# Kernel tuning notes

Measured on AMD Instinct MI355X. Metric: run time of the kernel, lower is better.

## Reference

```python
import jax, jax.numpy as jnp
import numpy as np

IN_DIM = 1024
OUT_DIM = 1024
QK_DIM = OUT_DIM // 4  # 256


def setup_inputs() -> dict:
    key = jax.random.key(0)
    kx, ky, kq, kk, kv = jax.random.split(key, 5)
    B, Sq, Sk = 16, 2048, 2048
    x = jax.random.normal(kx, (B, Sq, IN_DIM), dtype=jnp.float32)
    y = jax.random.normal(ky, (B, Sk, IN_DIM), dtype=jnp.float32)
    s = 1.0 / np.sqrt(IN_DIM)
    Wq = jax.random.normal(kq, (IN_DIM, QK_DIM), dtype=jnp.float32) * s
    Wk = jax.random.normal(kk, (IN_DIM, QK_DIM), dtype=jnp.float32) * s
    Wv = jax.random.normal(kv, (IN_DIM, OUT_DIM), dtype=jnp.float32) * s
    return {"x": x, "y": y, "Wq": Wq, "Wk": Wk, "Wv": Wv}


def reference(x, y, Wq, Wk, Wv):
    # q: [B,Sq,dk], k: [B,Sk,dk]
    q = jnp.einsum("bsd,dk->bsk", x, Wq)
    k = jnp.einsum("btd,dk->btk", y, Wk)
    # NOTE: original scales by out_dim**0.5, not qk dim
    scores = jnp.einsum("bsk,btk->bst", q, k) / jnp.sqrt(jnp.float32(OUT_DIM))
    attn = jax.nn.softmax(scores, axis=-1)
    v = jnp.einsum("btd,de->bte", y, Wv)
    out = jnp.einsum("bst,bte->bse", attn, v)
    return out + x
```

## Files before the change

kernel.cpp:

```cpp
#include <hip/hip_runtime.h>

typedef __attribute__((ext_vector_type(8))) short bf16x8;
typedef __attribute__((ext_vector_type(4))) short s16x4;
typedef __attribute__((ext_vector_type(4))) float f32x4;

#define MFMA16(a,b,c) __builtin_amdgcn_mfma_f32_16x16x32_bf16((a),(b),(c),0,0,0)

__device__ __forceinline__ unsigned short f2bf(float f) {
  unsigned int u = __float_as_uint(f);
  return (unsigned short)((u + 0x7fffu + ((u >> 16) & 1u)) >> 16);
}
__device__ __forceinline__ float bf2f(unsigned short u) {
  return __uint_as_float(((unsigned int)u) << 16);
}

__device__ __forceinline__ void gload16(const void* g, void* l) {
  __builtin_amdgcn_global_load_lds((const __attribute__((address_space(1))) void*)g,
                                   (__attribute__((address_space(3))) void*)l, 16, 0, 0);
}

__global__ __launch_bounds__(256) void cvt_bf16(const float* __restrict__ in,
                                                unsigned short* __restrict__ out, int n8) {
  for (int i = blockIdx.x * 256 + threadIdx.x; i < n8; i += gridDim.x * 256) {
    float4 a = ((const float4*)in)[2 * i];
    float4 b = ((const float4*)in)[2 * i + 1];
    s16x4 p0, p1;
    p0[0] = f2bf(a.x); p0[1] = f2bf(a.y); p0[2] = f2bf(a.z); p0[3] = f2bf(a.w);
    p1[0] = f2bf(b.x); p1[1] = f2bf(b.y); p1[2] = f2bf(b.z); p1[3] = f2bf(b.w);
    ((s16x4*)out)[2 * i] = p0;
    ((s16x4*)out)[2 * i + 1] = p1;
  }
}

__global__ __launch_bounds__(256) void tcvt(const float* __restrict__ W,
                                            unsigned short* __restrict__ Wt, int K, int N) {
  __shared__ float t[32][33];
  const int n0 = blockIdx.x * 32, k0 = blockIdx.y * 32;
  const int c = threadIdx.x & 31, r8 = threadIdx.x >> 5;
#pragma unroll
  for (int p = 0; p < 4; ++p) {
    int r = r8 + p * 8;
    t[r][c] = W[(size_t)(k0 + r) * N + n0 + c];
  }
  __syncthreads();
#pragma unroll
  for (int p = 0; p < 4; ++p) {
    int r = r8 + p * 8;
    Wt[(size_t)(n0 + r) * K + k0 + c] = f2bf(t[c][r]);
  }
}

__global__ __launch_bounds__(256) void proj_gemm(
    const unsigned short* __restrict__ A, const unsigned short* __restrict__ Bt,
    unsigned short* __restrict__ C, int N, int mode, float scale)
{
  __shared__ __align__(16) unsigned short As[2][4096];
  __shared__ __align__(16) unsigned short Bs[2][4096];
  const int tid = threadIdx.x, lane = tid & 63, w = tid >> 6;
  const int wr = w >> 1, wc = w & 1;
  const int lrow = lane & 15, lg = lane >> 4;
  const size_t bm = (size_t)blockIdx.x * 128;
  const size_t bn = (size_t)blockIdx.y * 128;
  const int rl = lane >> 2, cq = lane & 3;

  auto stage = [&](int kt, int buf) {
#pragma unroll
    for (int u = 0; u < 2; ++u) {
      int row = w * 32 + u * 16 + rl;
      gload16(A  + (bm + row) * 1024 + kt * 32 + cq * 8, &As[buf][(w * 32 + u * 16) * 32]);
      gload16(Bt + (bn + row) * 1024 + kt * 32 + cq * 8, &Bs[buf][(w * 32 + u * 16) * 32]);
    }
  };

  f32x4 acc[4][4] = {};
  stage(0, 0);
  __syncthreads();

  for (int kt = 0; kt < 32; ++kt) {
    const int cur = kt & 1;
    if (kt + 1 < 32) stage(kt + 1, cur ^ 1);
    bf16x8 af[4], bfr[4];
#pragma unroll
    for (int i = 0; i < 4; ++i)
      af[i] = *(const bf16x8*)&As[cur][(wr * 64 + i * 16 + lrow) * 32 + lg * 8];
#pragma unroll
    for (int j = 0; j < 4; ++j)
      bfr[j] = *(const bf16x8*)&Bs[cur][(wc * 64 + j * 16 + lrow) * 32 + lg * 8];
    __builtin_amdgcn_s_setprio(1);
#pragma unroll
    for (int i = 0; i < 4; ++i)
#pragma unroll
      for (int j = 0; j < 4; ++j)
        acc[i][j] = MFMA16(af[i], bfr[j], acc[i][j]);
    __builtin_amdgcn_s_setprio(0);
    __syncthreads();
  }

  const int orow0 = blockIdx.x * 128 + wr * 64;
  const int ocol0 = blockIdx.y * 128 + wc * 64;
  if (mode == 0) {
#pragma unroll
    for (int i = 0; i < 4; ++i)
#pragma unroll
      for (int j = 0; j < 4; ++j) {
        int col = ocol0 + j * 16 + lrow;
#pragma unroll
        for (int r = 0; r < 4; ++r) {
          int row = orow0 + i * 16 + lg * 4 + r;
          C[(size_t)row * N + col] = f2bf(acc[i][j][r] * scale);
        }
      }
  } else {
#pragma unroll
    for (int i = 0; i < 4; ++i) {
      int m0 = orow0 + i * 16 + lg * 4;
      int bb = m0 >> 11, t = m0 & 2047;
#pragma unroll
      for (int j = 0; j < 4; ++j) {
        int e = ocol0 + j * 16 + lrow;
        s16x4 pk;
#pragma unroll
        for (int r = 0; r < 4; ++r) pk[r] = (short)f2bf(acc[i][j][r]);
        *(s16x4*)(C + (size_t)bb * 2097152 + (size_t)e * 2048 + t) = pk;
      }
    }
  }
}

template<int NT, int NTIL, int MODE>
__global__ __launch_bounds__(512) void gemm8p(
    const unsigned short* __restrict__ Aall, const unsigned short* __restrict__ Ball,
    size_t abatch, size_t bbatch, int lda, int ldb,
    unsigned short* __restrict__ Cb, const float* __restrict__ X,
    float* __restrict__ Out, int b0, int nb)
{
  __shared__ __align__(16) unsigned short lds[65536];
  const int bid = blockIdx.x;
  const int bloc = bid % nb, tl = bid / nb;
  const int mtile = tl / NTIL, ntile = tl % NTIL;
  const int gb = b0 + bloc;
  const unsigned short* Ag = Aall + (MODE == 0 ? (size_t)gb : (size_t)bloc) * abatch
                                  + (size_t)mtile * 256 * lda;
  const unsigned short* Bg = Ball + (size_t)gb * bbatch + (size_t)ntile * 256 * ldb;

  const int tid = threadIdx.x, lane = tid & 63, w = tid >> 6;
  const int wm = w >> 2, wn = w & 3;
  const int lrow = lane & 15, lg = lane >> 4;
  char* lb = (char*)lds;

  auto stageU = [&](const unsigned short* G, int ld, int kofs, int ubyte) {
#pragma unroll
    for (int i = 0; i < 2; ++i) {
      int c = tid + 512 * i;
      int row = c >> 2, q = c & 3;
      int qs = q ^ ((row >> 1) & 3);
      gload16(G + (size_t)row * ld + kofs + qs * 8, lb + ubyte + c * 16);
    }
  };
  auto rdfrag = [&](int ubyte, int row) -> bf16x8 {
    return *(const bf16x8*)(lb + ubyte + row * 64 + ((lg ^ ((row >> 1) & 3)) << 4));
  };

  f32x4 acc[8][4] = {};
  bf16x8 af[8], bfr[2];

  stageU(Ag, lda, 0,  (0 * 2 + 0) * 16384);
  stageU(Bg, ldb, 0,  (1 * 2 + 0) * 16384);
  stageU(Ag, lda, 32, (2 * 2 + 0) * 16384);
  stageU(Bg, ldb, 32, (3 * 2 + 0) * 16384);
  stageU(Ag, lda, 64, (0 * 2 + 1) * 16384);
  stageU(Bg, ldb, 64, (1 * 2 + 1) * 16384);
  asm volatile("s_waitcnt vmcnt(8)" ::: "memory");
  __builtin_amdgcn_s_barrier();

  for (int T = 0; T < NT; ++T) {
    const int par = T & 1;
    const int a0b = (0 * 2 + par) * 16384, b0b = (1 * 2 + par) * 16384;
    const int a1b = (2 * 2 + par) * 16384, b1b = (3 * 2 + par) * 16384;

#pragma unroll
    for (int mf = 0; mf < 8; ++mf) af[mf] = rdfrag(a0b, wm * 128 + mf * 16 + lrow);
#pragma unroll
    for (int nf = 0; nf < 2; ++nf) bfr[nf] = rdfrag(b0b, wn * 64 + nf * 16 + lrow);
    if (T + 1 < NT) stageU(Ag, lda, (T + 1) * 64 + 32, (2 * 2 + ((T + 1) & 1)) * 16384);
    __builtin_amdgcn_s_barrier();
    asm volatile("s_waitcnt lgkmcnt(0)" ::: "memory");
    __builtin_amdgcn_sched_barrier(0);
    __builtin_amdgcn_s_setprio(1);
#pragma unroll
    for (int mf = 0; mf < 8; ++mf) {
      acc[mf][0] = MFMA16(af[mf], bfr[0], acc[mf][0]);
      acc[mf][1] = MFMA16(af[mf], bfr[1], acc[mf][1]);
    }
    __builtin_amdgcn_s_setprio(0);
    __builtin_amdgcn_s_barrier();

#pragma unroll
    for (int nf = 0; nf < 2; ++nf) bfr[nf] = rdfrag(b0b, wn * 64 + (nf + 2) * 16 + lrow);
    if (T + 1 < NT) stageU(Bg, ldb, (T + 1) * 64 + 32, (3 * 2 + ((T + 1) & 1)) * 16384);
    __builtin_amdgcn_s_barrier();
    asm volatile("s_waitcnt lgkmcnt(0)" ::: "memory");
    __builtin_amdgcn_sched_barrier(0);
    __builtin_amdgcn_s_setprio(1);
#pragma unroll
    for (int mf = 0; mf < 8; ++mf) {
      acc[mf][2] = MFMA16(af[mf], bfr[0], acc[mf][2]);
      acc[mf][3] = MFMA16(af[mf], bfr[1], acc[mf][3]);
    }
    __builtin_amdgcn_s_setprio(0);
    asm volatile("s_waitcnt vmcnt(8)" ::: "memory");
    __builtin_amdgcn_s_barrier();

#pragma unroll
    for (int mf = 0; mf < 8; ++mf) af[mf] = rdfrag(a1b, wm * 128 + mf * 16 + lrow);
#pragma unroll
    for (int nf = 0; nf < 2; ++nf) bfr[nf] = rdfrag(b1b, wn * 64 + (nf + 2) * 16 + lrow);
    if (T + 2 < NT) stageU(Ag, lda, (T + 2) * 64, (0 * 2 + par) * 16384);
    __builtin_amdgcn_s_barrier();
    asm volatile("s_waitcnt lgkmcnt(0)" ::: "memory");
    __builtin_amdgcn_sched_barrier(0);
    __builtin_amdgcn_s_setprio(1);
#pragma unroll
    for (int mf = 0; mf < 8; ++mf) {
      acc[mf][2] = MFMA16(af[mf], bfr[0], acc[mf][2]);
      acc[mf][3] = MFMA16(af[mf], bfr[1], acc[mf][3]);
    }
    __builtin_amdgcn_s_setprio(0);
    __builtin_amdgcn_s_barrier();

#pragma unroll
    for (int nf = 0; nf < 2; ++nf) bfr[nf] = rdfrag(b1b, wn * 64 + nf * 16 + lrow);
    if (T + 2 < NT) stageU(Bg, ldb, (T + 2) * 64, (1 * 2 + par) * 16384);
    __builtin_amdgcn_s_barrier();
    asm volatile("s_waitcnt lgkmcnt(0)" ::: "memory");
    __builtin_amdgcn_sched_barrier(0);
    __builtin_amdgcn_s_setprio(1);
#pragma unroll
    for (int mf = 0; mf < 8; ++mf) {
      acc[mf][0] = MFMA16(af[mf], bfr[0], acc[mf][0]);
      acc[mf][1] = MFMA16(af[mf], bfr[1], acc[mf][1]);
    }
    __builtin_amdgcn_s_setprio(0);
    asm volatile("s_waitcnt vmcnt(8)" ::: "memory");
    __builtin_amdgcn_s_barrier();
  }

  if (MODE == 0) {
    unsigned short* Cp = Cb + (size_t)bloc * 2048 * 2048;
#pragma unroll
    for (int mf = 0; mf < 8; ++mf)
#pragma unroll
      for (int r = 0; r < 4; ++r) {
        int row = mtile * 256 + wm * 128 + mf * 16 + lg * 4 + r;
#pragma unroll
        for (int nf = 0; nf < 4; ++nf) {
          int col = ntile * 256 + wn * 64 + nf * 16 + lrow;
          Cp[(size_t)row * 2048 + col] = f2bf(acc[mf][nf][r]);
        }
      }
  } else {
#pragma unroll
    for (int mf = 0; mf < 8; ++mf)
#pragma unroll
      for (int r = 0; r < 4; ++r) {
        int row = mtile * 256 + wm * 128 + mf * 16 + lg * 4 + r;
        const float* xr = X   + ((size_t)gb * 2048 + row) * 1024;
        float*      orp = Out + ((size_t)gb * 2048 + row) * 1024;
#pragma unroll
        for (int nf = 0; nf < 4; ++nf) {
          int col = ntile * 256 + wn * 64 + nf * 16 + lrow;
          orp[col] = acc[mf][nf][r] + xr[col];
        }
      }
  }
}

__global__ __launch_bounds__(256) void softmax_kernel(unsigned short* __restrict__ Sp) {
  const int row = blockIdx.x * 4 + (threadIdx.x >> 6);
  const int lane = threadIdx.x & 63;
  unsigned short* rp = Sp + (size_t)row * 2048;
  bf16x8 raw[4];
#pragma unroll
  for (int c = 0; c < 4; ++c) raw[c] = *(const bf16x8*)(rp + c * 512 + lane * 8);
  float v[32];
#pragma unroll
  for (int c = 0; c < 4; ++c)
#pragma unroll
    for (int j = 0; j < 8; ++j) v[c * 8 + j] = bf2f((unsigned short)raw[c][j]);
  float mx = v[0];
#pragma unroll
  for (int j = 1; j < 32; ++j) mx = fmaxf(mx, v[j]);
  mx = fmaxf(mx, __shfl_xor(mx, 1));
  mx = fmaxf(mx, __shfl_xor(mx, 2));
  mx = fmaxf(mx, __shfl_xor(mx, 4));
  mx = fmaxf(mx, __shfl_xor(mx, 8));
  mx = fmaxf(mx, __shfl_xor(mx, 16));
  mx = fmaxf(mx, __shfl_xor(mx, 32));
  float sum = 0.f;
#pragma unroll
  for (int j = 0; j < 32; ++j) { v[j] = __expf(v[j] - mx); sum += v[j]; }
  sum += __shfl_xor(sum, 1);
  sum += __shfl_xor(sum, 2);
  sum += __shfl_xor(sum, 4);
  sum += __shfl_xor(sum, 8);
  sum += __shfl_xor(sum, 16);
  sum += __shfl_xor(sum, 32);
  float inv = 1.0f / sum;
#pragma unroll
  for (int c = 0; c < 4; ++c) {
    bf16x8 pk;
#pragma unroll
    for (int j = 0; j < 8; ++j) pk[j] = (short)f2bf(v[c * 8 + j] * inv);
    *(bf16x8*)(rp + c * 512 + lane * 8) = pk;
  }
}

extern "C" void kernel_launch(void* const* d_in, const int* in_sizes, int n_in,
                              void* d_out, int out_size, void* d_ws, size_t ws_size,
                              hipStream_t stream) {
  (void)in_sizes; (void)n_in; (void)out_size;
  const float* x  = (const float*)d_in[0];
  const float* y  = (const float*)d_in[1];
  const float* Wq = (const float*)d_in[2];
  const float* Wk = (const float*)d_in[3];
  const float* Wv = (const float*)d_in[4];
  float* out = (float*)d_out;

  unsigned short* xb = (unsigned short*)d_out;
  unsigned short* yb = xb + (size_t)16 * 2048 * 1024;

  unsigned short* Wqt = (unsigned short*)d_ws;
  unsigned short* Wkt = Wqt + (size_t)256 * 1024;
  unsigned short* Wvt = Wkt + (size_t)256 * 1024;
  unsigned short* qws = Wvt + (size_t)1024 * 1024;
  unsigned short* kws = qws + (size_t)16 * 2048 * 256;
  unsigned short* vtw = kws + (size_t)16 * 2048 * 256;
  unsigned short* Sp  = vtw + (size_t)16 * 1024 * 2048;

  const size_t fixed_bytes = (size_t)(Sp - Wqt) * 2;
  const size_t s_batch_bytes = (size_t)2048 * 2048 * 2;
  int nb = 1;
  if      (ws_size >= fixed_bytes + 16 * s_batch_bytes) nb = 16;
  else if (ws_size >= fixed_bytes + 8  * s_batch_bytes) nb = 8;
  else if (ws_size >= fixed_bytes + 4  * s_batch_bytes) nb = 4;
  else if (ws_size >= fixed_bytes + 2  * s_batch_bytes) nb = 2;
  else nb = 1;

  const int n8 = (16 * 2048 * 1024) / 8;
  cvt_bf16<<<2048, 256, 0, stream>>>(x, xb, n8);
  cvt_bf16<<<2048, 256, 0, stream>>>(y, yb, n8);
  tcvt<<<dim3(8, 32),  256, 0, stream>>>(Wq, Wqt, 1024, 256);
  tcvt<<<dim3(8, 32),  256, 0, stream>>>(Wk, Wkt, 1024, 256);
  tcvt<<<dim3(32, 32), 256, 0, stream>>>(Wv, Wvt, 1024, 1024);

  proj_gemm<<<dim3(256, 2), 256, 0, stream>>>(xb, Wqt, qws, 256, 0, 0.03125f);
  proj_gemm<<<dim3(256, 2), 256, 0, stream>>>(yb, Wkt, kws, 256, 0, 1.0f);
  proj_gemm<<<dim3(256, 8), 256, 0, stream>>>(yb, Wvt, vtw, 1024, 2, 1.0f);

  for (int b0 = 0; b0 < 16; b0 += nb) {
    gemm8p<4, 8, 0><<<nb * 64, 512, 0, stream>>>(
        qws, kws, (size_t)2048 * 256, (size_t)2048 * 256, 256, 256,
        Sp, nullptr, nullptr, b0, nb);
    softmax_kernel<<<nb * 512, 256, 0, stream>>>(Sp);
    gemm8p<32, 4, 1><<<nb * 32, 512, 0, stream>>>(
        Sp, vtw, (size_t)2048 * 2048, (size_t)1024 * 2048, 2048, 2048,
        nullptr, x, out, b0, nb);
  }
}
```

Baseline: 532.9 us.

## Restructure GEMM main loop into 4-phase 4x4 MFMA blocks with prefetched fragments

```diff
diff --git a/kernel.cpp b/kernel.cpp
--- a/kernel.cpp
+++ b/kernel.cpp
@@ -127,8 +127,10 @@
   }
 }
 
+#define SBAR  do { __builtin_amdgcn_s_barrier(); __builtin_amdgcn_sched_barrier(0); } while (0)
+
 template<int NT, int NTIL, int MODE>
-__global__ __launch_bounds__(512) void gemm8p(
+__global__ __launch_bounds__(512) void gemm4p(
     const unsigned short* __restrict__ Aall, const unsigned short* __restrict__ Ball,
     size_t abatch, size_t bbatch, int lda, int ldb,
     unsigned short* __restrict__ Cb, const float* __restrict__ X,
@@ -162,7 +164,7 @@
   };
 
   f32x4 acc[8][4] = {};
-  bf16x8 af[8], bfr[2];
+  bf16x8 afA[4], afB[4], bfrA[4], bfrB[4];
 
   stageU(Ag, lda, 0,  (0 * 2 + 0) * 16384);
   stageU(Bg, ldb, 0,  (1 * 2 + 0) * 16384);
@@ -171,78 +173,80 @@
   stageU(Ag, lda, 64, (0 * 2 + 1) * 16384);
   stageU(Bg, ldb, 64, (1 * 2 + 1) * 16384);
   asm volatile("s_waitcnt vmcnt(8)" ::: "memory");
-  __builtin_amdgcn_s_barrier();
+  SBAR;
+#pragma unroll
+  for (int i = 0; i < 4; ++i) afA[i] = rdfrag(0, wm * 128 + i * 16 + lrow);
+#pragma unroll
+  for (int nf = 0; nf < 4; ++nf) bfrA[nf] = rdfrag(2 * 16384, wn * 64 + nf * 16 + lrow);
 
   for (int T = 0; T < NT; ++T) {
-    const int par = T & 1;
-    const int a0b = (0 * 2 + par) * 16384, b0b = (1 * 2 + par) * 16384;
-    const int a1b = (2 * 2 + par) * 16384, b1b = (3 * 2 + par) * 16384;
-
-#pragma unroll
-    for (int mf = 0; mf < 8; ++mf) af[mf] = rdfrag(a0b, wm * 128 + mf * 16 + lrow);
-#pragma unroll
-    for (int nf = 0; nf < 2; ++nf) bfr[nf] = rdfrag(b0b, wn * 64 + nf * 16 + lrow);
-    if (T + 1 < NT) stageU(Ag, lda, (T + 1) * 64 + 32, (2 * 2 + ((T + 1) & 1)) * 16384);
-    __builtin_amdgcn_s_barrier();
-    asm volatile("s_waitcnt lgkmcnt(0)" ::: "memory");
+    const int pc = T & 1, pn = (T + 1) & 1;
+    const int a0b = (0 * 2 + pc) * 16384, b0b = (1 * 2 + pc) * 16384;
+    const int a1b = (2 * 2 + pc) * 16384, b1b = (3 * 2 + pc) * 16384;
+    const int t1 = (T + 1 < NT) ? T + 1 : 0;
+    const int t2 = (T + 2 < NT) ? T + 2 : 0;
+
+#pragma unroll
+    for (int i = 0; i < 4; ++i) afB[i] = rdfrag(a0b, wm * 128 + (i + 4) * 16 + lrow);
+    stageU(Ag, lda, t1 * 64 + 32, (2 * 2 + pn) * 16384);
+    asm volatile("s_waitcnt lgkmcnt(4)" ::: "memory");
     __builtin_amdgcn_sched_barrier(0);
     __builtin_amdgcn_s_setprio(1);
 #pragma unroll
-    for (int mf = 0; mf < 8; ++mf) {
-      acc[mf][0] = MFMA16(af[mf], bfr[0], acc[mf][0]);
-      acc[mf][1] = MFMA16(af[mf], bfr[1], acc[mf][1]);
-    }
-    __builtin_amdgcn_s_setprio(0);
-    __builtin_amdgcn_s_barrier();
-
-#pragma unroll
-    for (int nf = 0; nf < 2; ++nf) bfr[nf] = rdfrag(b0b, wn * 64 + (nf + 2) * 16 + lrow);
-    if (T + 1 < NT) stageU(Bg, ldb, (T + 1) * 64 + 32, (3 * 2 + ((T + 1) & 1)) * 16384);
-    __builtin_amdgcn_s_barrier();
-    asm volatile("s_waitcnt lgkmcnt(0)" ::: "memory");
+    for (int mf = 0; mf < 4; ++mf)
+#pragma unroll
+      for (int nf = 0; nf < 4; ++nf)
+        acc[mf][nf] = MFMA16(afA[mf], bfrA[nf], acc[mf][nf]);
+    __builtin_amdgcn_s_setprio(0);
+    asm volatile("s_waitcnt vmcnt(6)" ::: "memory");
+    SBAR;
+
+#pragma unroll
+    for (int i = 0; i < 4; ++i) afA[i] = rdfrag(a1b, wm * 128 + i * 16 + lrow);
+#pragma unroll
+    for (int nf = 0; nf < 4; ++nf) bfrB[nf] = rdfrag(b1b, wn * 64 + nf * 16 + lrow);
+    stageU(Bg, ldb, t1 * 64 + 32, (3 * 2 + pn) * 16384);
+    asm volatile("s_waitcnt lgkmcnt(8)" ::: "memory");
     __builtin_amdgcn_sched_barrier(0);
     __builtin_amdgcn_s_setprio(1);
 #pragma unroll
-    for (int mf = 0; mf < 8; ++mf) {
-      acc[mf][2] = MFMA16(af[mf], bfr[0], acc[mf][2]);
-      acc[mf][3] = MFMA16(af[mf], bfr[1], acc[mf][3]);
-    }
-    __builtin_amdgcn_s_setprio(0);
-    asm volatile("s_waitcnt vmcnt(8)" ::: "memory");
-    __builtin_amdgcn_s_barrier();
-
-#pragma unroll
-    for (int mf = 0; mf < 8; ++mf) af[mf] = rdfrag(a1b, wm * 128 + mf * 16 + lrow);
-#pragma unroll
-    for (int nf = 0; nf < 2; ++nf) bfr[nf] = rdfrag(b1b, wn * 64 + (nf + 2) * 16 + lrow);
-    if (T + 2 < NT) stageU(Ag, lda, (T + 2) * 64, (0 * 2 + par) * 16384);
-    __builtin_amdgcn_s_barrier();
-    asm volatile("s_waitcnt lgkmcnt(0)" ::: "memory");
+    for (int mf = 0; mf < 4; ++mf)
+#pragma unroll
+      for (int nf = 0; nf < 4; ++nf)
+        acc[mf + 4][nf] = MFMA16(afB[mf], bfrA[nf], acc[mf + 4][nf]);
+    __builtin_amdgcn_s_setprio(0);
+    SBAR;
+
+#pragma unroll
+    for (int i = 0; i < 4; ++i) afB[i] = rdfrag(a1b, wm * 128 + (i + 4) * 16 + lrow);
+    stageU(Ag, lda, t2 * 64, (0 * 2 + pc) * 16384);
+    asm volatile("s_waitcnt lgkmcnt(4)" ::: "memory");
     __builtin_amdgcn_sched_barrier(0);
     __builtin_amdgcn_s_setprio(1);
 #pragma unroll
-    for (int mf = 0; mf < 8; ++mf) {
-      acc[mf][2] = MFMA16(af[mf], bfr[0], acc[mf][2]);
-      acc[mf][3] = MFMA16(af[mf], bfr[1], acc[mf][3]);
-    }
-    __builtin_amdgcn_s_setprio(0);
-    __builtin_amdgcn_s_barrier();
-
-#pragma unroll
-    for (int nf = 0; nf < 2; ++nf) bfr[nf] = rdfrag(b1b, wn * 64 + nf * 16 + lrow);
-    if (T + 2 < NT) stageU(Bg, ldb, (T + 2) * 64, (1 * 2 + par) * 16384);
-    __builtin_amdgcn_s_barrier();
-    asm volatile("s_waitcnt lgkmcnt(0)" ::: "memory");
+    for (int mf = 0; mf < 4; ++mf)
+#pragma unroll
+      for (int nf = 0; nf < 4; ++nf)
+        acc[mf][nf] = MFMA16(afA[mf], bfrB[nf], acc[mf][nf]);
+    __builtin_amdgcn_s_setprio(0);
+    asm volatile("s_waitcnt vmcnt(6)" ::: "memory");
+    SBAR;
+
+#pragma unroll
+    for (int i = 0; i < 4; ++i) afA[i] = rdfrag((0 * 2 + pn) * 16384, wm * 128 + i * 16 + lrow);
+#pragma unroll
+    for (int nf = 0; nf < 4; ++nf) bfrA[nf] = rdfrag((1 * 2 + pn) * 16384, wn * 64 + nf * 16 + lrow);
+    stageU(Bg, ldb, t2 * 64, (1 * 2 + pc) * 16384);
+    asm volatile("s_waitcnt lgkmcnt(8)" ::: "memory");
     __builtin_amdgcn_sched_barrier(0);
     __builtin_amdgcn_s_setprio(1);
 #pragma unroll
-    for (int mf = 0; mf < 8; ++mf) {
-      acc[mf][0] = MFMA16(af[mf], bfr[0], acc[mf][0]);
-      acc[mf][1] = MFMA16(af[mf], bfr[1], acc[mf][1]);
-    }
-    __builtin_amdgcn_s_setprio(0);
-    asm volatile("s_waitcnt vmcnt(8)" ::: "memory");
-    __builtin_amdgcn_s_barrier();
+    for (int mf = 0; mf < 4; ++mf)
+#pragma unroll
+      for (int nf = 0; nf < 4; ++nf)
+        acc[mf + 4][nf] = MFMA16(afB[mf], bfrB[nf], acc[mf + 4][nf]);
+    __builtin_amdgcn_s_setprio(0);
+    SBAR;
   }
 
   if (MODE == 0) {
@@ -358,11 +362,11 @@
   proj_gemm<<<dim3(256, 8), 256, 0, stream>>>(yb, Wvt, vtw, 1024, 2, 1.0f);
 
   for (int b0 = 0; b0 < 16; b0 += nb) {
-    gemm8p<4, 8, 0><<<nb * 64, 512, 0, stream>>>(
+    gemm4p<4, 8, 0><<<nb * 64, 512, 0, stream>>>(
         qws, kws, (size_t)2048 * 256, (size_t)2048 * 256, 256, 256,
         Sp, nullptr, nullptr, b0, nb);
     softmax_kernel<<<nb * 512, 256, 0, stream>>>(Sp);
-    gemm8p<32, 4, 1><<<nb * 32, 512, 0, stream>>>(
+    gemm4p<32, 4, 1><<<nb * 32, 512, 0, stream>>>(
         Sp, vtw, (size_t)2048 * 2048, (size_t)1024 * 2048, 2048, 2048,
         nullptr, x, out, b0, nb);
   }
```

Result: no change. 538.6 us (+1.1%).
